# Kernel optimization log

Measured on AMD Instinct MI355X. Metric: run time of the kernel, lower is better.

## Reference

```python
import jax, jax.numpy as jnp
import numpy as np

OUT_H, OUT_W = 7, 7          # pooled output size
SR = 2                        # sampling_ratio (samples per bin side)
SCALE = 0.25                  # spatial_scale (stride-4 FPN level)
EPS = 1e-8


def setup_inputs() -> dict:
    key = jax.random.key(0)
    k1, k2, k3, k4, k5, k6 = jax.random.split(key, 6)
    N, C, H, W = 2, 256, 200, 200
    R = 1000
    inp = jax.random.normal(k1, (N, C, H, W), dtype=jnp.float32)
    # rois: (batch_idx, x_ctr, y_ctr, width, height, angle_degrees) in image coords
    bidx = jax.random.randint(k2, (R,), 0, N).astype(jnp.float32)
    xc = jax.random.uniform(k3, (R,), minval=0.0, maxval=W / SCALE)
    yc = jax.random.uniform(k4, (R,), minval=0.0, maxval=H / SCALE)
    wh = jax.random.uniform(k5, (R, 2), minval=32.0, maxval=256.0)
    ang = jax.random.uniform(k6, (R,), minval=-90.0, maxval=90.0)
    rois = jnp.concatenate([bidx[:, None], xc[:, None], yc[:, None], wh, ang[:, None]], axis=1)
    return {"input": inp, "rois": rois}


def _roi_align_rotated(feat, rois):
    """Detectron2-style rotated RoIAlign (aligned, continuous coords).
    feat: [N,C,H,W] float; rois: [R,6] -> out [R,C,OUT_H,OUT_W]."""
    N, C, H, W = feat.shape
    R = rois.shape[0]
    b = rois[:, 0].astype(jnp.int32)
    cw = rois[:, 1] * SCALE - 0.5          # roi center (continuous pixel coords)
    ch = rois[:, 2] * SCALE - 0.5
    rw = jnp.maximum(rois[:, 3] * SCALE, 1.0)
    rh = jnp.maximum(rois[:, 4] * SCALE, 1.0)
    theta = rois[:, 5] * jnp.float32(np.pi / 180.0)
    cos_t, sin_t = jnp.cos(theta), jnp.sin(theta)

    bin_h = rh / OUT_H
    bin_w = rw / OUT_W
    # sample offsets within each bin: (i + 0.5)/SR for i in [0, SR)
    frac = (jnp.arange(SR, dtype=feat.dtype) + 0.5) / SR
    # local (un-rotated) coords relative to roi center: [R, OUT, SR]
    yy = (-rh / 2)[:, None, None] + (jnp.arange(OUT_H, dtype=feat.dtype)[None, :, None] + frac[None, None, :]) * bin_h[:, None, None]
    xx = (-rw / 2)[:, None, None] + (jnp.arange(OUT_W, dtype=feat.dtype)[None, :, None] + frac[None, None, :]) * bin_w[:, None, None]
    # rotate into feature-map coords: [R, PH, PW, GH, GW]
    yy5 = yy[:, :, None, :, None]
    xx5 = xx[:, None, :, None, :]
    c5 = cos_t[:, None, None, None, None]
    s5 = sin_t[:, None, None, None, None]
    y = yy5 * c5 - xx5 * s5 + ch[:, None, None, None, None]
    x = yy5 * s5 + xx5 * c5 + cw[:, None, None, None, None]

    S = OUT_H * OUT_W * SR * SR
    y = y.reshape(R, S)
    x = x.reshape(R, S)

    valid = (y >= -1.0) & (y <= H) & (x >= -1.0) & (x <= W)
    y = jnp.maximum(y, 0.0)
    x = jnp.maximum(x, 0.0)
    yl0 = jnp.floor(y).astype(jnp.int32)
    xl0 = jnp.floor(x).astype(jnp.int32)
    cy = yl0 >= H - 1
    cx = xl0 >= W - 1
    y_low = jnp.where(cy, H - 1, yl0)
    y_high = jnp.where(cy, H - 1, yl0 + 1)
    yv = jnp.where(cy, jnp.asarray(H - 1, feat.dtype), y)
    x_low = jnp.where(cx, W - 1, xl0)
    x_high = jnp.where(cx, W - 1, xl0 + 1)
    xv = jnp.where(cx, jnp.asarray(W - 1, feat.dtype), x)

    ly = yv - y_low.astype(feat.dtype)
    lx = xv - x_low.astype(feat.dtype)
    hy, hx = 1.0 - ly, 1.0 - lx
    w1, w2, w3, w4 = hy * hx, hy * lx, ly * hx, ly * lx

    bb = b[:, None]  # [R,1] broadcast against [R,S]
    v1 = feat[bb, :, y_low, x_low]    # [R,S,C]
    v2 = feat[bb, :, y_low, x_high]
    v3 = feat[bb, :, y_high, x_low]
    v4 = feat[bb, :, y_high, x_high]
    val = (w1[..., None] * v1 + w2[..., None] * v2
           + w3[..., None] * v3 + w4[..., None] * v4)
    val = jnp.where(valid[..., None], val, 0.0)
    # average over the SR*SR samples in each bin
    out = val.reshape(R, OUT_H, OUT_W, SR * SR, C).sum(axis=3) / (SR * SR)
    return out.transpose(0, 3, 1, 2)  # [R,C,PH,PW]


def reference(input, rois):
    out = _roi_align_rotated(input, rois)
    # wrapper applies torch.nan_to_num(roi_align, EPS, EPS, EPS)
    return jnp.nan_to_num(out, nan=EPS, posinf=EPS, neginf=EPS)
```

## Files before the change

kernel.cpp:

```cpp
#include <hip/hip_runtime.h>
#include <hip/hip_fp16.h>

#define FH 200
#define FW 200
#define FHW 40000
#define FC 256
#define NBIN 49
#define NSAMP 196
#define OH_STRIDE 136

__device__ __forceinline__ void compute_sample(const float* __restrict__ roi,
                                               int s, bool nhwc,
                                               float4* wout, int4* oout)
{
    int   b  = (int)roi[0];
    float cw = roi[1] * 0.25f - 0.5f;
    float ch = roi[2] * 0.25f - 0.5f;
    float rw = fmaxf(roi[3] * 0.25f, 1.0f);
    float rh = fmaxf(roi[4] * 0.25f, 1.0f);
    float th = roi[5] * 0.017453292519943295f;
    float ct = cosf(th);
    float st = sinf(th);
    float bin_h = rh / 7.0f;
    float bin_w = rw / 7.0f;

    int bin = s >> 2;
    int sub = s & 3;
    int iy  = sub >> 1;
    int ix  = sub & 1;
    int ph  = bin / 7;
    int pw  = bin - ph * 7;

    float fy = 0.25f + 0.5f * (float)iy;
    float fx = 0.25f + 0.5f * (float)ix;
    float yy = -rh * 0.5f + ((float)ph + fy) * bin_h;
    float xx = -rw * 0.5f + ((float)pw + fx) * bin_w;
    float y  = yy * ct - xx * st + ch;
    float x  = yy * st + xx * ct + cw;

    bool valid = (y >= -1.0f) && (y <= (float)FH) && (x >= -1.0f) && (x <= (float)FW);
    y = fmaxf(y, 0.0f);
    x = fmaxf(x, 0.0f);
    int y0 = (int)floorf(y);
    int x0 = (int)floorf(x);
    bool cy = (y0 >= FH - 1);
    bool cx = (x0 >= FW - 1);
    int ylo = cy ? (FH - 1) : y0;
    int yhi = cy ? (FH - 1) : (y0 + 1);
    int xlo = cx ? (FW - 1) : x0;
    int xhi = cx ? (FW - 1) : (x0 + 1);
    float ly = cy ? 0.0f : (y - (float)y0);
    float lx = cx ? 0.0f : (x - (float)x0);
    float hy = 1.0f - ly;
    float hx = 1.0f - lx;
    float m  = valid ? 0.25f : 0.0f;

    *wout = make_float4(hy * hx * m, hy * lx * m, ly * hx * m, ly * lx * m);

    int bb = b * (FC * FHW);
    int p0 = ylo * FW + xlo;
    int p1 = ylo * FW + xhi;
    int p2 = yhi * FW + xlo;
    int p3 = yhi * FW + xhi;
    if (nhwc)
        *oout = make_int4(bb + p0 * FC, bb + p1 * FC, bb + p2 * FC, bb + p3 * FC);
    else
        *oout = make_int4(bb + p0, bb + p1, bb + p2, bb + p3);
}

__device__ __forceinline__ float fixnum(float v)
{
    return (v == v && v <= 3.402823466e38f && v >= -3.402823466e38f) ? v : 1e-8f;
}

__global__ __launch_bounds__(256)
void transpose_f16_kernel(const float* __restrict__ in, __half* __restrict__ out)
{
    __shared__ __align__(16) __half tileT[32][72];
    int b   = blockIdx.z;
    int p0  = blockIdx.x * 32;
    int c0  = blockIdx.y * 64;
    int tid = threadIdx.x;

    const float* inb  = in  + (size_t)b * FC * FHW;
    __half*      outb = out + (size_t)b * FHW * FC;

#pragma unroll
    for (int k = 0; k < 2; ++k) {
        int chl = k * 32 + (tid >> 3);
        int px4 = (tid & 7) * 4;
        float4 v = *(const float4*)(inb + (size_t)(c0 + chl) * FHW + p0 + px4);
        int g   = ((chl >> 3) ^ (px4 >> 2)) & 7;
        int col = (g << 3) | (chl & 7);
        tileT[px4 + 0][col] = __float2half(v.x);
        tileT[px4 + 1][col] = __float2half(v.y);
        tileT[px4 + 2][col] = __float2half(v.z);
        tileT[px4 + 3][col] = __float2half(v.w);
    }
    __syncthreads();

    int p = tid >> 3;
    int q = tid & 7;
    int g = (q ^ ((p >> 2) & 7));
    uint4 d = *(const uint4*)&tileT[p][g << 3];
    *(uint4*)(outb + (size_t)(p0 + p) * FC + c0 + q * 8) = d;
}

__global__ __launch_bounds__(256)
void roi_nhwc_f16_kernel(const __half* __restrict__ feat,
                         const float* __restrict__ rois,
                         float* __restrict__ out)
{
    __shared__ float4 s_w[NSAMP];
    __shared__ int4   s_o[NSAMP];
    __shared__ __align__(16) __half out_h[NBIN * OH_STRIDE];

    int r   = blockIdx.x;
    int c0  = blockIdx.y * 128;
    int tid = threadIdx.x;

    const float* roi = rois + r * 6;
    if (tid < NSAMP) {
        float4 w; int4 o;
        compute_sample(roi, tid, true, &w, &o);
        s_w[tid] = w;
        s_o[tid] = o;
    }
    __syncthreads();

    int grp    = tid >> 4;
    int lane16 = tid & 15;
    int ch8    = lane16 * 8;

    const __half* fbase = feat + c0 + ch8;

    for (int bin = grp; bin < NBIN; bin += 16) {
        float acc[8];
#pragma unroll
        for (int i = 0; i < 8; ++i) acc[i] = 0.0f;

#pragma unroll
        for (int sub = 0; sub < 4; ++sub) {
            int s = bin * 4 + sub;
            float4 wt = s_w[s];
            int4   o  = s_o[s];
            uint4 u0 = *(const uint4*)(fbase + o.x);
            uint4 u1 = *(const uint4*)(fbase + o.y);
            uint4 u2 = *(const uint4*)(fbase + o.z);
            uint4 u3 = *(const uint4*)(fbase + o.w);
            const __half2* h0 = (const __half2*)&u0;
            const __half2* h1 = (const __half2*)&u1;
            const __half2* h2 = (const __half2*)&u2;
            const __half2* h3 = (const __half2*)&u3;
#pragma unroll
            for (int j = 0; j < 4; ++j) {
                float2 f0 = __half22float2(h0[j]);
                float2 f1 = __half22float2(h1[j]);
                float2 f2 = __half22float2(h2[j]);
                float2 f3 = __half22float2(h3[j]);
                acc[2 * j + 0] += wt.x * f0.x + wt.y * f1.x + wt.z * f2.x + wt.w * f3.x;
                acc[2 * j + 1] += wt.x * f0.y + wt.y * f1.y + wt.z * f2.y + wt.w * f3.y;
            }
        }
        __half2 hv[4];
#pragma unroll
        for (int j = 0; j < 4; ++j)
            hv[j] = __floats2half2_rn(acc[2 * j + 0], acc[2 * j + 1]);
        *(uint4*)&out_h[bin * OH_STRIDE + ch8] = *(const uint4*)hv;
    }
    __syncthreads();

    float* obase = out + (size_t)r * (FC * NBIN) + (size_t)blockIdx.y * (128 * NBIN);
    for (int v4 = tid; v4 < (128 * NBIN) / 4; v4 += 256) {
        int f0 = v4 * 4;
        float vals[4];
#pragma unroll
        for (int i = 0; i < 4; ++i) {
            int f = f0 + i;
            int c = f / NBIN;
            int b = f - c * NBIN;
            vals[i] = fixnum(__half2float(out_h[b * OH_STRIDE + c]));
        }
        *(float4*)(obase + f0) = make_float4(vals[0], vals[1], vals[2], vals[3]);
    }
}

__global__ __launch_bounds__(256)
void roi_nchw_kernel(const float* __restrict__ feat,
                     const float* __restrict__ rois,
                     float* __restrict__ out)
{
    int r   = blockIdx.x;
    int tid = threadIdx.x;

    __shared__ float4 s_w[NSAMP];
    __shared__ int4   s_o[NSAMP];

    const float* roi = rois + r * 6;
    if (tid < NSAMP) {
        float4 w; int4 o;
        compute_sample(roi, tid, false, &w, &o);
        s_w[tid] = w;
        s_o[tid] = o;
    }
    __syncthreads();

    const float* fc = feat + (size_t)tid * FHW;
    float* obase = out + (size_t)r * (FC * NBIN) + (size_t)tid * NBIN;

    for (int bin = 0; bin < NBIN; ++bin) {
        float a = 0.0f;
#pragma unroll
        for (int k = 0; k < 4; ++k) {
            float4 w = s_w[bin * 4 + k];
            int4   o = s_o[bin * 4 + k];
            a += w.x * fc[o.x] + w.y * fc[o.y] + w.z * fc[o.z] + w.w * fc[o.w];
        }
        obase[bin] = fixnum(a);
    }
}

extern "C" void kernel_launch(void* const* d_in, const int* in_sizes, int n_in,
                              void* d_out, int out_size, void* d_ws, size_t ws_size,
                              hipStream_t stream)
{
    const float* feat = (const float*)d_in[0];
    const float* rois = (const float*)d_in[1];
    float* out = (float*)d_out;

    int R = in_sizes[1] / 6;
    int N = in_sizes[0] / (FC * FHW);
    size_t need = (size_t)in_sizes[0] * sizeof(__half);

    if (ws_size >= need) {
        __half* featT = (__half*)d_ws;
        dim3 tg(FHW / 32, FC / 64, N);
        transpose_f16_kernel<<<tg, 256, 0, stream>>>(feat, featT);
        dim3 g(R, 2, 1);
        roi_nhwc_f16_kernel<<<g, 256, 0, stream>>>(featT, rois, out);
    } else {
        roi_nchw_kernel<<<R, 256, 0, stream>>>(feat, rois, out);
    }
}
```

Measured before the change: 175.5 us.

## Split ROI blocks into four channel quarters with grouped block ordering

Each ROI is now handled by four blocks of 64 channels instead of two blocks of 128, on a 1D grid that interleaves 8 ROIs by 4 channel quarters. The goal is more parallelism and better L2 locality, since consecutive blocks gather from the same ROI's feature pixels. In exchange, the per-block sample-weight setup (trig and offsets) is duplicated twice as often. The shared staging buffer uses a smaller, unaligned stride with half2 stores in place of 16-byte stores, and 32 bin groups leave a partial second pass over the 49 bins.

```diff
diff --git a/kernel.cpp b/kernel.cpp
--- a/kernel.cpp
+++ b/kernel.cpp
@@ -7,7 +7,7 @@
 #define FC 256
 #define NBIN 49
 #define NSAMP 196
-#define OH_STRIDE 136
+#define OHS 66
 
 __device__ __forceinline__ void compute_sample(const float* __restrict__ roi,
                                                int s, bool nhwc,
@@ -109,14 +109,17 @@
 __global__ __launch_bounds__(256)
 void roi_nhwc_f16_kernel(const __half* __restrict__ feat,
                          const float* __restrict__ rois,
-                         float* __restrict__ out)
+                         float* __restrict__ out, int R)
 {
     __shared__ float4 s_w[NSAMP];
     __shared__ int4   s_o[NSAMP];
-    __shared__ __align__(16) __half out_h[NBIN * OH_STRIDE];
-
-    int r   = blockIdx.x;
-    int c0  = blockIdx.y * 128;
+    __shared__ __half out_h[NBIN * OHS];
+
+    int l = blockIdx.x;
+    int r = (l >> 5) * 8 + (l & 7);
+    int q = (l >> 3) & 3;
+    if (r >= R) return;
+    int c0  = q * 64;
     int tid = threadIdx.x;
 
     const float* roi = rois + r * 6;
@@ -128,13 +131,13 @@
     }
     __syncthreads();
 
-    int grp    = tid >> 4;
-    int lane16 = tid & 15;
-    int ch8    = lane16 * 8;
+    int grp   = tid >> 3;
+    int lane8 = tid & 7;
+    int ch8   = lane8 * 8;
 
     const __half* fbase = feat + c0 + ch8;
 
-    for (int bin = grp; bin < NBIN; bin += 16) {
+    for (int bin = grp; bin < NBIN; bin += 32) {
         float acc[8];
 #pragma unroll
         for (int i = 0; i < 8; ++i) acc[i] = 0.0f;
@@ -162,16 +165,15 @@
                 acc[2 * j + 1] += wt.x * f0.y + wt.y * f1.y + wt.z * f2.y + wt.w * f3.y;
             }
         }
-        __half2 hv[4];
+        __half2* dst = (__half2*)&out_h[bin * OHS + ch8];
 #pragma unroll
         for (int j = 0; j < 4; ++j)
-            hv[j] = __floats2half2_rn(acc[2 * j + 0], acc[2 * j + 1]);
-        *(uint4*)&out_h[bin * OH_STRIDE + ch8] = *(const uint4*)hv;
-    }
-    __syncthreads();
-
-    float* obase = out + (size_t)r * (FC * NBIN) + (size_t)blockIdx.y * (128 * NBIN);
-    for (int v4 = tid; v4 < (128 * NBIN) / 4; v4 += 256) {
+            dst[j] = __floats2half2_rn(acc[2 * j + 0], acc[2 * j + 1]);
+    }
+    __syncthreads();
+
+    float* obase = out + (size_t)r * (FC * NBIN) + (size_t)c0 * NBIN;
+    for (int v4 = tid; v4 < (64 * NBIN) / 4; v4 += 256) {
         int f0 = v4 * 4;
         float vals[4];
 #pragma unroll
@@ -179,7 +181,7 @@
             int f = f0 + i;
             int c = f / NBIN;
             int b = f - c * NBIN;
-            vals[i] = fixnum(__half2float(out_h[b * OH_STRIDE + c]));
+            vals[i] = fixnum(__half2float(out_h[b * OHS + c]));
         }
         *(float4*)(obase + f0) = make_float4(vals[0], vals[1], vals[2], vals[3]);
     }
@@ -236,8 +238,8 @@
         __half* featT = (__half*)d_ws;
         dim3 tg(FHW / 32, FC / 64, N);
         transpose_f16_kernel<<<tg, 256, 0, stream>>>(feat, featT);
-        dim3 g(R, 2, 1);
-        roi_nhwc_f16_kernel<<<g, 256, 0, stream>>>(featT, rois, out);
+        int nblk = ((R + 7) / 8) * 32;
+        roi_nhwc_f16_kernel<<<nblk, 256, 0, stream>>>(featT, rois, out, R);
     } else {
         roi_nchw_kernel<<<R, 256, 0, stream>>>(feat, rois, out);
     }
```

Result: slower. 179.2 us (+2.1%).
